# Kernel tuning notes

Measured on AMD Instinct MI355X. Metric: run time of the kernel, lower is better.

Reference implementation:

```python
import jax, jax.numpy as jnp
import numpy as np

BLOCK = 32          # MX_BLOCK_SIZE
SCALE_EMAX = 127.0  # scale_bits=8 -> shared exponent clamped to [-127, 127]


def _quantize_elem(x, ebits, mfrac, max_norm):
    """Quantize each element to a tiny float format (ebits exponent bits,
    mfrac fractional mantissa bits), round-half-to-even, saturate to max_norm."""
    ax = jnp.abs(x)
    priv = jnp.floor(jnp.log2(jnp.where(ax == 0, 1.0, ax)))
    min_exp = float(-(2 ** (ebits - 1)) + 2)  # subnormal flush exponent
    priv = jnp.maximum(priv, min_exp)
    scale = jnp.exp2(priv - mfrac)
    q = jnp.round(x / scale) * scale  # jnp.round is round-half-to-even
    return jnp.clip(q, -max_norm, max_norm)


def _quantize_mx(x, ebits, mfrac, emax_elem, max_norm):
    """MX block-floating-point quantization along the last axis.
    shared_exp = floor(log2(blockmax)) - emax_elem (shared_exp_method='max')."""
    shp = x.shape
    xb = x.reshape(shp[:-1] + (shp[-1] // BLOCK, BLOCK))
    amax = jnp.max(jnp.abs(xb), axis=-1, keepdims=True)
    sexp = jnp.floor(jnp.log2(jnp.where(amax == 0, 1.0, amax))) - emax_elem
    sexp = jnp.clip(sexp, -SCALE_EMAX, SCALE_EMAX)
    scale = jnp.exp2(sexp)
    q = _quantize_elem(xb / scale, ebits, mfrac, max_norm) * scale
    return q.reshape(shp)


def _q_act(x):
    # fp6_e2m3: ebits=2, 3 fractional mantissa bits, emax=2, max_norm=7.5
    return _quantize_mx(x, 2, 3.0, 2.0, 7.5)


def _q_w(w):
    # fp4_e2m1: ebits=2, 1 fractional mantissa bit, emax=2, max_norm=6.0
    return _quantize_mx(w, 2, 1.0, 2.0, 6.0)


def _mx_linear(x, w):
    # quantize activation (fp6) and weight (fp4) along the shared in_features axis,
    # then do the matmul in high precision (dequant-fused GEMM semantics).
    return jnp.einsum('bsh,oh->bso', _q_act(x), _q_w(w))


def setup_inputs() -> dict:
    key = jax.random.key(0)
    k1, k2, k3, k4 = jax.random.split(key, 4)
    B, S, H, I = 1, 4096, 2048, 8192
    x = jax.random.normal(k1, (B, S, H), dtype=jnp.float32)
    w_gate = jax.random.normal(k2, (I, H), dtype=jnp.float32) * 0.02
    w_up = jax.random.normal(k3, (I, H), dtype=jnp.float32) * 0.02
    w_down = jax.random.normal(k4, (H, I), dtype=jnp.float32) * 0.02
    return {"x": x, "w_gate": w_gate, "w_up": w_up, "w_down": w_down}


def reference(x, w_gate, w_up, w_down):
    gate = _mx_linear(x, w_gate)            # [B, S, I]
    up = _mx_linear(x, w_up)                # [B, S, I]
    inter = jax.nn.silu(gate) * up          # SwiGLU
    return _mx_linear(inter, w_down)        # [B, S, H]
```

## Files before the change

### kernel.cpp

```cpp
#include <hip/hip_runtime.h>
#include <hip/hip_bf16.h>

typedef __attribute__((ext_vector_type(4))) int i32x4;
typedef __attribute__((ext_vector_type(8))) int i32x8;
typedef __attribute__((ext_vector_type(4))) float f32x4;

__device__ __forceinline__ int flog2(float x) {
  unsigned u = __float_as_uint(x);
  int e = (int)((u >> 23) & 255u);
  if (e) return e - 127;
  unsigned m = u & 0x7fffffu;
  return (31 - __clz(m)) - 149;
}

__device__ __forceinline__ float exp2i(int e) {
  int e1 = e >> 1, e2 = e - e1;
  return __uint_as_float((unsigned)(e1 + 127) << 23) *
         __uint_as_float((unsigned)(e2 + 127) << 23);
}

template <int MFRAC>
__device__ __forceinline__ float qelem(float y, float maxn) {
  float ay = fabsf(y);
  int e = (ay == 0.f) ? 0 : flog2(ay);
  if (e < 0) e = 0;
  float r = rintf(y * exp2i(MFRAC - e)) * exp2i(e - MFRAC);
  return fminf(fmaxf(r, -maxn), maxn);
}

__device__ __forceinline__ unsigned char enc_rne(float v) {
  unsigned u = __float_as_uint(v);
  unsigned s = u >> 31;
  float a = fabsf(v);
  if (a == 0.f) return (unsigned char)(s << 7);
  int e = flog2(a);
  if (e < -6) e = -6;
  int qi = (int)rintf(a * exp2i(3 - e));
  if (qi == 0) return (unsigned char)(s << 7);
  if (qi == 16) { qi = 8; e += 1; }
  unsigned exf, m;
  if (qi < 8) { exf = 0u; m = (unsigned)qi; }
  else { exf = (unsigned)(e + 7); m = (unsigned)(qi - 8); }
  return (unsigned char)((s << 7) | (exf << 3) | m);
}

__device__ __forceinline__ size_t swz(int row, int col, int pa) {
  return ((size_t)((row >> 4) * pa + (col >> 7))) * 2048
       + (size_t)(((col >> 4) & 1) * 1024
       + ((row & 15) + ((col >> 5) & 3) * 16) * 16
       + (col & 15));
}

template <int MFRAC, int EMAX>
__global__ void quant_fold(const float* __restrict__ in, unsigned char* __restrict__ out,
                           long n4, float maxn, int se0, int kshift, int kmask, int pa) {
  long i = (long)blockIdx.x * blockDim.x + threadIdx.x;
  long stride = (long)gridDim.x * blockDim.x;
  for (; i < n4; i += stride) {
    float4 v = reinterpret_cast<const float4*>(in)[i];
    float am = fmaxf(fmaxf(fabsf(v.x), fabsf(v.y)), fmaxf(fabsf(v.z), fabsf(v.w)));
    am = fmaxf(am, __shfl_xor(am, 1));
    am = fmaxf(am, __shfl_xor(am, 2));
    am = fmaxf(am, __shfl_xor(am, 4));
    int se = ((am == 0.f) ? 0 : flog2(am)) - EMAX;
    se = se < -127 ? -127 : (se > 127 ? 127 : se);
    float inv = exp2i(-se), f = exp2i(se - se0);
    unsigned o = (unsigned)enc_rne(qelem<MFRAC>(v.x * inv, maxn) * f)
               | ((unsigned)enc_rne(qelem<MFRAC>(v.y * inv, maxn) * f) << 8)
               | ((unsigned)enc_rne(qelem<MFRAC>(v.z * inv, maxn) * f) << 16)
               | ((unsigned)enc_rne(qelem<MFRAC>(v.w * inv, maxn) * f) << 24);
    int row = (int)(i >> kshift);
    int kq = ((int)i & kmask) * 4;
    reinterpret_cast<unsigned*>(out)[swz(row, kq, pa) >> 2] = o;
  }
}

__device__ __forceinline__ i32x8 gfrag(const unsigned char* page, int l16) {
  i32x4 lo = *reinterpret_cast<const i32x4*>(page + l16);
  i32x4 hi = *reinterpret_cast<const i32x4*>(page + 1024 + l16);
  i32x8 r;
  r[0] = lo[0]; r[1] = lo[1]; r[2] = lo[2]; r[3] = lo[3];
  r[4] = hi[0]; r[5] = hi[1]; r[6] = hi[2]; r[7] = hi[3];
  return r;
}

template <int EPI>
__global__ __launch_bounds__(256, 2) void mx_gemm(
    const unsigned char* __restrict__ A, int pa,
    const unsigned char* __restrict__ B, int pb,
    float* __restrict__ Cf, float* __restrict__ Cf2,
    const float* __restrict__ gate, unsigned char* __restrict__ C8,
    int W, int K, int ldC, int c0, float fac, int se0out, int nby, int nks) {
  const int t = threadIdx.x, l = t & 63, w = t >> 6;
  const int wr = w >> 1, wc = w & 1;
  const int lr16 = l & 15, lg16 = l >> 4;
  const int l16 = l * 16;
  const int n = (int)blockIdx.x;
  const int bx = n & 31, byks = n >> 5;
  const int by = byks % nby, ks = byks / nby;
  const int rowA = bx * 128, rowB = by * 256;
  const int kbs = ks * (K >> 7);
  const int SCL = 0x7f7f7f7f;

  f32x4 acc[4][8];
#pragma unroll
  for (int i = 0; i < 4; ++i)
#pragma unroll
    for (int j = 0; j < 8; ++j) acc[i][j] = (f32x4)(0.f);

  const unsigned char* pApg[4];
  const unsigned char* pBpg[8];
#pragma unroll
  for (int m = 0; m < 4; ++m)
    pApg[m] = A + ((size_t)((rowA >> 4) + wr * 4 + m) * pa + kbs) * 2048;
#pragma unroll
  for (int nn = 0; nn < 8; ++nn)
    pBpg[nn] = B + ((size_t)((rowB >> 4) + wc * 8 + nn) * pb + kbs) * 2048;

  const int nt = K >> 7;
#pragma unroll 2
  for (int kb = 0; kb < nt; ++kb) {
    i32x8 af[4], bf[8];
#pragma unroll
    for (int m = 0; m < 4; ++m) { af[m] = gfrag(pApg[m], l16); pApg[m] += 2048; }
#pragma unroll
    for (int nn = 0; nn < 8; ++nn) { bf[nn] = gfrag(pBpg[nn], l16); pBpg[nn] += 2048; }
#pragma unroll
    for (int m = 0; m < 4; ++m)
#pragma unroll
      for (int nn = 0; nn < 8; ++nn)
        acc[m][nn] = __builtin_amdgcn_mfma_scale_f32_16x16x128_f8f6f4(
            af[m], bf[nn], acc[m][nn], 0, 0, 0, SCL, 0, SCL);
  }

  if (EPI == 0) {
    float* D = ks ? Cf2 : Cf;
#pragma unroll
    for (int m = 0; m < 4; ++m)
#pragma unroll
      for (int nn = 0; nn < 8; ++nn)
#pragma unroll
        for (int r = 0; r < 4; ++r) {
          int row = rowA + wr * 64 + m * 16 + lg16 * 4 + r;
          int col = rowB + wc * 128 + nn * 16 + lr16;
          D[(size_t)row * ldC + c0 + col] = acc[m][nn][r] * fac;
        }
  } else {
    const int pao = ldC >> 7;
#pragma unroll
    for (int m = 0; m < 4; ++m)
#pragma unroll
      for (int p = 0; p < 4; ++p)
#pragma unroll
        for (int r = 0; r < 4; ++r) {
          int row = rowA + wr * 64 + m * 16 + lg16 * 4 + r;
          int col = rowB + wc * 128 + p * 32 + lr16;
          float u0 = acc[m][2 * p][r] * fac;
          float u1 = acc[m][2 * p + 1][r] * fac;
          float g0 = gate[(size_t)row * W + col];
          float g1 = gate[(size_t)row * W + col + 16];
          float v0 = u0 * (g0 / (1.f + expf(-g0)));
          float v1 = u1 * (g1 / (1.f + expf(-g1)));
          float am = fmaxf(fabsf(v0), fabsf(v1));
          am = fmaxf(am, __shfl_xor(am, 1));
          am = fmaxf(am, __shfl_xor(am, 2));
          am = fmaxf(am, __shfl_xor(am, 4));
          am = fmaxf(am, __shfl_xor(am, 8));
          int se = ((am == 0.f) ? 0 : flog2(am)) - 2;
          se = se < -127 ? -127 : (se > 127 ? 127 : se);
          float f = exp2i(-se), fo = exp2i(se - se0out);
          C8[swz(row, c0 + col, pao)] = enc_rne(qelem<3>(v0 * f, 7.5f) * fo);
          C8[swz(row, c0 + col + 16, pao)] = enc_rne(qelem<3>(v1 * f, 7.5f) * fo);
        }
  }
}

__global__ void add_f32(float* __restrict__ out, const float* __restrict__ part, long n4) {
  long i = (long)blockIdx.x * blockDim.x + threadIdx.x;
  long stride = (long)gridDim.x * blockDim.x;
  for (; i < n4; i += stride) {
    float4 a = reinterpret_cast<float4*>(out)[i];
    float4 b = reinterpret_cast<const float4*>(part)[i];
    a.x += b.x; a.y += b.y; a.z += b.z; a.w += b.w;
    reinterpret_cast<float4*>(out)[i] = a;
  }
}

extern "C" void kernel_launch(void* const* d_in, const int* in_sizes, int n_in,
                              void* d_out, int out_size, void* d_ws, size_t ws_size,
                              hipStream_t stream) {
  const float* x = (const float*)d_in[0];
  const float* wg = (const float*)d_in[1];
  const float* wu = (const float*)d_in[2];
  const float* wd = (const float*)d_in[3];
  float* out = (float*)d_out;

  const int S = 4096, H = 2048, I = 8192;

  const int SE0X = -1, SE0W = -7, SE0I = -2;
  const float FAC_GU = 0.00390625f;
  const float FAC_DN = 0.001953125f;

  unsigned char* p = (unsigned char*)d_ws;
  unsigned char* xq8 = p;  p += (size_t)S * H;
  unsigned char* wgq8 = p; p += (size_t)I * H;
  unsigned char* wuq8 = p; p += (size_t)I * H;
  unsigned char* wdq8 = p; p += (size_t)H * I;
  unsigned char* iq8 = p;  p += (size_t)S * I;
  size_t base_bytes = (size_t)(p - (unsigned char*)d_ws);
  float* gatef = (float*)p;
  float* pf = (float*)p;

  quant_fold<3, 2><<<2048, 256, 0, stream>>>(x, xq8, (long)S * H / 4, 7.5f, SE0X,
                                             9, 511, H / 128);
  quant_fold<1, 2><<<2048, 256, 0, stream>>>(wg, wgq8, (long)I * H / 4, 6.0f, SE0W,
                                             9, 511, H / 128);
  quant_fold<1, 2><<<2048, 256, 0, stream>>>(wu, wuq8, (long)I * H / 4, 6.0f, SE0W,
                                             9, 511, H / 128);
  quant_fold<1, 2><<<2048, 256, 0, stream>>>(wd, wdq8, (long)H * I / 4, 6.0f, SE0W,
                                             11, 2047, I / 128);

  size_t avail = ws_size > base_bytes ? ws_size - base_bytes : 0;
  int W = 256;
  for (int cand = I; cand >= 256; cand >>= 1)
    if ((size_t)S * cand * 4 <= avail) { W = cand; break; }

  for (int c0 = 0; c0 < I; c0 += W) {
    int nby = W / 256;
    mx_gemm<0><<<32 * nby, 256, 0, stream>>>(
        xq8, H / 128, wgq8 + (size_t)c0 * H, H / 128, gatef, nullptr,
        nullptr, nullptr, W, H, W, 0, FAC_GU, 0, nby, 1);
    mx_gemm<1><<<32 * nby, 256, 0, stream>>>(
        xq8, H / 128, wuq8 + (size_t)c0 * H, H / 128, nullptr, nullptr,
        gatef, iq8, W, H, I, c0, FAC_GU, SE0I, nby, 1);
  }

  mx_gemm<0><<<32 * (H / 256) * 2, 256, 0, stream>>>(
      iq8, I / 128, wdq8, I / 128, out, pf, nullptr, nullptr,
      H, I / 2, H, 0, FAC_DN, 0, H / 256, 2);
  add_f32<<<2048, 256, 0, stream>>>(out, pf, (long)S * H / 4);
}
```

Before: 501.3 us.

## Fuse gate and up GEMMs into one kernel with in-register SwiGLU epilogue

Replaces the separate gate GEMM (writing fp32 gate to workspace) and up GEMM (reading it back) with a single kernel that computes both gate and up accumulators for a 128x128 tile and applies SiLU, multiply and fp6 requantization directly from registers. This removes a large fp32 intermediate write and read (S x I floats) and one kernel launch per chunk. In exchange the per-block tile shrinks to 128 columns with two accumulator sets, which changes A-fragment reuse and register pressure.

```diff
diff --git a/kernel.cpp b/kernel.cpp
--- a/kernel.cpp
+++ b/kernel.cpp
@@ -84,13 +84,89 @@
   return r;
 }
 
-template <int EPI>
-__global__ __launch_bounds__(256, 2) void mx_gemm(
+__global__ __launch_bounds__(256, 2) void mx_gateup(
+    const unsigned char* __restrict__ A, int pa,
+    const unsigned char* __restrict__ Bg, const unsigned char* __restrict__ Bu, int pb,
+    unsigned char* __restrict__ C8, int ldC, float fac, int se0out, int nby) {
+  const int t = threadIdx.x, l = t & 63, w = t >> 6;
+  const int wr = w >> 1, wc = w & 1;
+  const int lr16 = l & 15, lg16 = l >> 4;
+  const int l16 = l * 16;
+  const int n = (int)blockIdx.x;
+  const int bx = n % 32, by = n / 32;
+  const int rowA = bx * 128, rowB = by * 128;
+  const int SCL = 0x7f7f7f7f;
+
+  f32x4 accg[4][4], accu[4][4];
+#pragma unroll
+  for (int i = 0; i < 4; ++i)
+#pragma unroll
+    for (int j = 0; j < 4; ++j) { accg[i][j] = (f32x4)(0.f); accu[i][j] = (f32x4)(0.f); }
+
+  const unsigned char* pApg[4];
+  const unsigned char* pBg[4];
+  const unsigned char* pBu[4];
+#pragma unroll
+  for (int m = 0; m < 4; ++m) {
+    pApg[m] = A + (size_t)((rowA >> 4) + wr * 4 + m) * pa * 2048;
+    pBg[m] = Bg + (size_t)((rowB >> 4) + wc * 4 + m) * pb * 2048;
+    pBu[m] = Bu + (size_t)((rowB >> 4) + wc * 4 + m) * pb * 2048;
+  }
+
+  const int nt = pa;
+#pragma unroll 2
+  for (int kb = 0; kb < nt; ++kb) {
+    i32x8 af[4], bg[4], bu[4];
+#pragma unroll
+    for (int m = 0; m < 4; ++m) { af[m] = gfrag(pApg[m], l16); pApg[m] += 2048; }
+#pragma unroll
+    for (int m = 0; m < 4; ++m) { bg[m] = gfrag(pBg[m], l16); pBg[m] += 2048; }
+#pragma unroll
+    for (int m = 0; m < 4; ++m) { bu[m] = gfrag(pBu[m], l16); pBu[m] += 2048; }
+#pragma unroll
+    for (int m = 0; m < 4; ++m)
+#pragma unroll
+      for (int nn = 0; nn < 4; ++nn) {
+        accg[m][nn] = __builtin_amdgcn_mfma_scale_f32_16x16x128_f8f6f4(
+            af[m], bg[nn], accg[m][nn], 0, 0, 0, SCL, 0, SCL);
+        accu[m][nn] = __builtin_amdgcn_mfma_scale_f32_16x16x128_f8f6f4(
+            af[m], bu[nn], accu[m][nn], 0, 0, 0, SCL, 0, SCL);
+      }
+  }
+
+  const int pao = ldC >> 7;
+#pragma unroll
+  for (int m = 0; m < 4; ++m)
+#pragma unroll
+    for (int p = 0; p < 2; ++p)
+#pragma unroll
+      for (int r = 0; r < 4; ++r) {
+        int row = rowA + wr * 64 + m * 16 + lg16 * 4 + r;
+        int col = rowB + wc * 64 + p * 32 + lr16;
+        float g0 = accg[m][2 * p][r] * fac;
+        float g1 = accg[m][2 * p + 1][r] * fac;
+        float u0 = accu[m][2 * p][r] * fac;
+        float u1 = accu[m][2 * p + 1][r] * fac;
+        float v0 = u0 * (g0 / (1.f + expf(-g0)));
+        float v1 = u1 * (g1 / (1.f + expf(-g1)));
+        float am = fmaxf(fabsf(v0), fabsf(v1));
+        am = fmaxf(am, __shfl_xor(am, 1));
+        am = fmaxf(am, __shfl_xor(am, 2));
+        am = fmaxf(am, __shfl_xor(am, 4));
+        am = fmaxf(am, __shfl_xor(am, 8));
+        int se = ((am == 0.f) ? 0 : flog2(am)) - 2;
+        se = se < -127 ? -127 : (se > 127 ? 127 : se);
+        float f = exp2i(-se), fo = exp2i(se - se0out);
+        C8[swz(row, col, pao)] = enc_rne(qelem<3>(v0 * f, 7.5f) * fo);
+        C8[swz(row, col + 16, pao)] = enc_rne(qelem<3>(v1 * f, 7.5f) * fo);
+      }
+}
+
+__global__ __launch_bounds__(256, 2) void mx_down(
     const unsigned char* __restrict__ A, int pa,
     const unsigned char* __restrict__ B, int pb,
     float* __restrict__ Cf, float* __restrict__ Cf2,
-    const float* __restrict__ gate, unsigned char* __restrict__ C8,
-    int W, int K, int ldC, int c0, float fac, int se0out, int nby, int nks) {
+    int K, int ldC, float fac, int nby) {
   const int t = threadIdx.x, l = t & 63, w = t >> 6;
   const int wr = w >> 1, wc = w & 1;
   const int lr16 = l & 15, lg16 = l >> 4;
@@ -133,46 +209,17 @@
             af[m], bf[nn], acc[m][nn], 0, 0, 0, SCL, 0, SCL);
   }
 
-  if (EPI == 0) {
-    float* D = ks ? Cf2 : Cf;
-#pragma unroll
-    for (int m = 0; m < 4; ++m)
-#pragma unroll
-      for (int nn = 0; nn < 8; ++nn)
-#pragma unroll
-        for (int r = 0; r < 4; ++r) {
-          int row = rowA + wr * 64 + m * 16 + lg16 * 4 + r;
-          int col = rowB + wc * 128 + nn * 16 + lr16;
-          D[(size_t)row * ldC + c0 + col] = acc[m][nn][r] * fac;
-        }
-  } else {
-    const int pao = ldC >> 7;
-#pragma unroll
-    for (int m = 0; m < 4; ++m)
-#pragma unroll
-      for (int p = 0; p < 4; ++p)
-#pragma unroll
-        for (int r = 0; r < 4; ++r) {
-          int row = rowA + wr * 64 + m * 16 + lg16 * 4 + r;
-          int col = rowB + wc * 128 + p * 32 + lr16;
-          float u0 = acc[m][2 * p][r] * fac;
-          float u1 = acc[m][2 * p + 1][r] * fac;
-          float g0 = gate[(size_t)row * W + col];
-          float g1 = gate[(size_t)row * W + col + 16];
-          float v0 = u0 * (g0 / (1.f + expf(-g0)));
-          float v1 = u1 * (g1 / (1.f + expf(-g1)));
-          float am = fmaxf(fabsf(v0), fabsf(v1));
-          am = fmaxf(am, __shfl_xor(am, 1));
-          am = fmaxf(am, __shfl_xor(am, 2));
-          am = fmaxf(am, __shfl_xor(am, 4));
-          am = fmaxf(am, __shfl_xor(am, 8));
-          int se = ((am == 0.f) ? 0 : flog2(am)) - 2;
-          se = se < -127 ? -127 : (se > 127 ? 127 : se);
-          float f = exp2i(-se), fo = exp2i(se - se0out);
-          C8[swz(row, c0 + col, pao)] = enc_rne(qelem<3>(v0 * f, 7.5f) * fo);
-          C8[swz(row, c0 + col + 16, pao)] = enc_rne(qelem<3>(v1 * f, 7.5f) * fo);
-        }
-  }
+  float* D = ks ? Cf2 : Cf;
+#pragma unroll
+  for (int m = 0; m < 4; ++m)
+#pragma unroll
+    for (int nn = 0; nn < 8; ++nn)
+#pragma unroll
+      for (int r = 0; r < 4; ++r) {
+        int row = rowA + wr * 64 + m * 16 + lg16 * 4 + r;
+        int col = rowB + wc * 128 + nn * 16 + lr16;
+        D[(size_t)row * ldC + col] = acc[m][nn][r] * fac;
+      }
 }
 
 __global__ void add_f32(float* __restrict__ out, const float* __restrict__ part, long n4) {
@@ -207,8 +254,6 @@
   unsigned char* wuq8 = p; p += (size_t)I * H;
   unsigned char* wdq8 = p; p += (size_t)H * I;
   unsigned char* iq8 = p;  p += (size_t)S * I;
-  size_t base_bytes = (size_t)(p - (unsigned char*)d_ws);
-  float* gatef = (float*)p;
   float* pf = (float*)p;
 
   quant_fold<3, 2><<<2048, 256, 0, stream>>>(x, xq8, (long)S * H / 4, 7.5f, SE0X,
@@ -220,23 +265,10 @@
   quant_fold<1, 2><<<2048, 256, 0, stream>>>(wd, wdq8, (long)H * I / 4, 6.0f, SE0W,
                                              11, 2047, I / 128);
 
-  size_t avail = ws_size > base_bytes ? ws_size - base_bytes : 0;
-  int W = 256;
-  for (int cand = I; cand >= 256; cand >>= 1)
-    if ((size_t)S * cand * 4 <= avail) { W = cand; break; }
-
-  for (int c0 = 0; c0 < I; c0 += W) {
-    int nby = W / 256;
-    mx_gemm<0><<<32 * nby, 256, 0, stream>>>(
-        xq8, H / 128, wgq8 + (size_t)c0 * H, H / 128, gatef, nullptr,
-        nullptr, nullptr, W, H, W, 0, FAC_GU, 0, nby, 1);
-    mx_gemm<1><<<32 * nby, 256, 0, stream>>>(
-        xq8, H / 128, wuq8 + (size_t)c0 * H, H / 128, nullptr, nullptr,
-        gatef, iq8, W, H, I, c0, FAC_GU, SE0I, nby, 1);
-  }
-
-  mx_gemm<0><<<32 * (H / 256) * 2, 256, 0, stream>>>(
-      iq8, I / 128, wdq8, I / 128, out, pf, nullptr, nullptr,
-      H, I / 2, H, 0, FAC_DN, 0, H / 256, 2);
+  mx_gateup<<<32 * (I / 128), 256, 0, stream>>>(
+      xq8, H / 128, wgq8, wuq8, H / 128, iq8, I, FAC_GU, SE0I, I / 128);
+
+  mx_down<<<32 * (H / 256) * 2, 256, 0, stream>>>(
+      iq8, I / 128, wdq8, I / 128, out, pf, I / 2, H, FAC_DN, H / 256);
   add_f32<<<2048, 256, 0, stream>>>(out, pf, (long)S * H / 4);
 }
```

New measurement: 415.2 us. -17.2%, faster.
